# Kernel tuning notes

Hardware: AMD Instinct MI355X
Metric: run time of the kernel (lower is better)

Reference implementation:

```python
import jax, jax.numpy as jnp
import numpy as np

B, P, V = 8, 16, 32
N_TH1 = 20
N_TH2 = 2 * (N_TH1 - 1) + 1
NPC, NNS, NOUT = 16384, 8192, 8192


def make_directions(n_th1):
    n_th2 = 2 * (n_th1 - 1) + 1
    th1 = np.linspace(-np.pi / 2, np.pi / 2, n_th1)
    th2 = np.linspace(-np.pi, np.pi, n_th2)
    c1, s1 = np.cos(th1), np.sin(th1)
    c2, s2 = np.cos(th2), np.sin(th2)
    ds = []
    for i in range(1, n_th1 - 1):
        for j in range(n_th2 - 1):
            ds.append([c1[i] * c2[j], c1[i] * s2[j], s1[i]])
    ds.append([c1[0] * c2[0], c1[0] * s2[0], s1[0]])
    ds.append([c1[-1] * c2[0], c1[-1] * s2[0], s1[-1]])
    return np.asarray(ds, np.float32)

DIRS = jnp.asarray(make_directions(N_TH1))
D = DIRS.shape[0]  # (n_th1-2)*(n_th2-1)+2 = 686


def _spt(dirs, verts, smooth, trans):
    # dirs [B,P,N,3], verts [B,P,V,3] (centered), trans [B,P,1,3]
    z = jnp.einsum('bpvc,bpnc->bpvn', verts, dirs)          # [B,P,V,N]
    zm = jnp.maximum(z, 0.0)
    pe = smooth[:, :, None, None]                            # [B,P,1,1]
    maxz = jnp.clip(jnp.max(z, axis=2, keepdims=True), 1e-30, 1e30)
    k = 1.0 / maxz                                           # [B,P,1,N]
    zmk = jnp.clip(zm * k, 1e-30, 1e30)                      # tiny floor keeps pow grads finite
    sum_zm_p = jnp.sum(zmk ** pe, axis=2, keepdims=True)     # [B,P,1,N]
    h = sum_zm_p ** (1.0 / pe)                               # normalized support value
    s = jnp.clip(h, 1e-30, 1e30)
    dhdz = jnp.clip((zmk / s) ** (pe - 1.0), 1e-30, 1e30)    # [B,P,V,N]
    surf = jnp.einsum('bpvn,bpvc->bpnc', dhdz, verts) + trans
    h_out = jnp.clip(h / k, -1e30, 1e30).transpose(0, 1, 3, 2)  # [B,P,N,1]
    return h_out, surf


def _distance(verts, smooth, trans, pts, normal_filter=None):
    # pts [B,P,N,3]: per-part query points in global coords
    local = pts - trans
    nrm = jnp.sqrt(jnp.clip(jnp.sum(local * local, -1, keepdims=True), 1e-40, 1e40))
    d = local / nrm                                          # unit directions [B,P,N,3]
    h, surf = _spt(d, verts, smooth, trans)
    dist = nrm - h                                           # signed distance to support plane
    if normal_filter is not None:
        dist = jnp.where(normal_filter, 100.0, dist)
    return dist, surf, d


def _overlap(verts, smooth, trans):
    t = trans[:, :, 0, :]                                    # [B,P,3]
    diff = t[:, None, :, :] - t[:, :, None, :]               # [B,i,j,3] = t_j - t_i
    dn = jnp.sqrt(jnp.clip(jnp.sum(diff * diff, -1, keepdims=True), 1e-20, 1e20))
    eyem = jnp.eye(t.shape[1], dtype=t.dtype)[None, :, :, None]
    safe = jnp.array([1.0, 0.0, 0.0], dtype=t.dtype)
    d = diff / dn * (1.0 - eyem) + eyem * safe               # safe diagonal direction
    h, _ = _spt(d, verts, smooth, trans)                     # [B,P,P,1] support of part i toward j
    sep = dn - h - jnp.swapaxes(h, 1, 2)                     # center gap minus both supports
    return jax.nn.relu(-sep) * (1.0 - eyem)


def _forward(vertices, smoothness, pointcloud, nearsurf, out):
    mean_v = jnp.mean(vertices, axis=2, keepdims=True)       # [B,P,1,3]
    local_v = vertices - mean_v
    x = jnp.broadcast_to(DIRS[None, None], (B, P, D, 3))
    h, _ = _spt(x, local_v, smoothness, mean_v)              # [B,P,D,1]
    overlap = _overlap(local_v, smoothness, mean_v)
    pc = jnp.broadcast_to(pointcloud[:, None], (B, P, NPC, 3))
    distance, _, _ = _distance(local_v, smoothness, mean_v, pc)
    scale = jnp.clip(jnp.max(h, axis=2, keepdims=True), 1e-10, 10.0)  # [B,P,1,1]
    _, surf_pts, normals = _distance(local_v, smoothness, mean_v, x * scale + mean_v)
    surf_points = surf_pts.reshape(B, P * D, 3)
    sp2 = jnp.broadcast_to(surf_points[:, None], (B, P, P * D, 3))
    local_trans = jnp.transpose(mean_v, (0, 2, 1, 3)) - mean_v        # [B,P,P,3]
    nf = jnp.einsum('bijc,bidc->bijd', local_trans, normals)          # [B,P,P,D]
    normal_filter = nf.reshape(B, P, P * D)[..., None] < 0
    surf_distance, _, _ = _distance(local_v, smoothness, mean_v, sp2, normal_filter=normal_filter)
    sd = surf_distance.reshape(B, P, P, D, 1)
    df = 100.0 * jnp.eye(P, dtype=sd.dtype)[None, :, :, None, None]
    sd = jnp.where(df > 0, df, sd)                           # mask self-distance
    surf_distance = sd.reshape(B, P, P * D, 1)
    ns = jnp.broadcast_to(nearsurf[:, None], (B, P, NNS, 3))
    nearsurf_dist, _, _ = _distance(local_v, smoothness, mean_v, ns)
    op = jnp.broadcast_to(out[:, None], (B, P, NOUT, 3))
    out_dist, _, _ = _distance(local_v, smoothness, mean_v, op)
    return overlap, distance, x, surf_distance, surf_points, nearsurf_dist, out_dist


def setup_inputs() -> dict:
    key = jax.random.key(0)
    k1, k2, k3, k4, k5, k6 = jax.random.split(key, 6)
    centers = jax.random.uniform(k1, (B, P, 1, 3), minval=-1.0, maxval=1.0)
    vertices = centers + 0.3 * jax.random.normal(k2, (B, P, V, 3))
    smoothness = 2.5 + 7.5 * jax.random.uniform(k3, (B, P))
    pointcloud = jax.random.uniform(k4, (B, NPC, 3), minval=-1.5, maxval=1.5)
    nearsurf = jax.random.uniform(k5, (B, NNS, 3), minval=-1.5, maxval=1.5)
    out = jax.random.uniform(k6, (B, NOUT, 3), minval=-2.0, maxval=2.0)
    return {"vertices": vertices, "smoothness": smoothness, "pointcloud": pointcloud,
            "nearsurf": nearsurf, "out": out}


def reference(vertices, smoothness, pointcloud, nearsurf, out):
    return _forward(vertices, smoothness, pointcloud, nearsurf, out)
```

## Files before the change

kernel.cpp:

```cpp
#include <hip/hip_runtime.h>
#include <math.h>

#define PP 16
#define VV 32
#define DD 686

__device__ __forceinline__ float clampf(float x, float lo, float hi) {
    return fminf(fmaxf(x, lo), hi);
}
__device__ __forceinline__ float fexp2(float x) { return __builtin_amdgcn_exp2f(x); }
__device__ __forceinline__ float flog2(float x) { return __builtin_amdgcn_logf(x); }
__device__ __forceinline__ float frsq (float x) { return __builtin_amdgcn_rsqf(x); }
__device__ __forceinline__ float zpow(float z, float pe) {
    return fexp2(pe * flog2(fmaxf(z, 1e-30f)));
}

__device__ __forceinline__ float spt_h4(const float4* __restrict__ sv4, float pe, float ipe,
                                        float lx, float ly, float lz)
{
    float s0 = 0.f, s1 = 0.f, s2 = 0.f, s3 = 0.f;
#pragma unroll
    for (int c = 0; c < 8; ++c) {
        float4 a = sv4[3*c+0], b = sv4[3*c+1], d = sv4[3*c+2];
        s0 += zpow(a.x*lx + a.y*ly + a.z*lz, pe);
        s1 += zpow(a.w*lx + b.x*ly + b.y*lz, pe);
        s2 += zpow(b.z*lx + b.w*ly + d.x*lz, pe);
        s3 += zpow(d.y*lx + d.z*ly + d.w*lz, pe);
    }
    return fexp2(flog2((s0+s1) + (s2+s3)) * ipe);
}

__global__ void k_setup(const float* __restrict__ verts, const float* __restrict__ smooth,
                        double* __restrict__ dmean, float* __restrict__ fmean,
                        float* __restrict__ flocal, float* __restrict__ fpe,
                        float* __restrict__ finvpe, float* __restrict__ fdirs,
                        int BP, int doDirs)
{
    int blk = blockIdx.x;
    int tid = threadIdx.x;
    if (blk < 3) {
        if (!doDirs) return;
        int idx = blk * 256 + tid;
        if (idx >= DD) return;
        int i, j;
        if (idx < 684)      { i = idx / 38 + 1; j = idx - (idx / 38) * 38; }
        else if (idx == 684){ i = 0;  j = 0; }
        else                { i = 19; j = 0; }
        const double pi = 3.14159265358979323846;
        double th1 = -pi * 0.5 + (double)i * (pi / 19.0);
        double th2 = -pi       + (double)j * (pi / 19.0);
        fdirs[3*idx+0] = (float)(cos(th1) * cos(th2));
        fdirs[3*idx+1] = (float)(cos(th1) * sin(th2));
        fdirs[3*idx+2] = (float)(sin(th1));
        return;
    }
    int bp = (blk - 3) * 256 + tid;
    if (bp >= BP) return;
    const float* vv = verts + (size_t)bp * VV * 3;
    double sx = 0.0, sy = 0.0, sz = 0.0;
#pragma unroll
    for (int k = 0; k < VV; ++k) {
        sx += (double)vv[3*k+0];
        sy += (double)vv[3*k+1];
        sz += (double)vv[3*k+2];
    }
    double mx = sx / 32.0, my = sy / 32.0, mz = sz / 32.0;
    dmean[3*bp+0] = mx; dmean[3*bp+1] = my; dmean[3*bp+2] = mz;
    fmean[3*bp+0] = (float)mx; fmean[3*bp+1] = (float)my; fmean[3*bp+2] = (float)mz;
    float* lv = flocal + (size_t)bp * VV * 3;
#pragma unroll
    for (int k = 0; k < VV; ++k) {
        lv[3*k+0] = (float)((double)vv[3*k+0] - mx);
        lv[3*k+1] = (float)((double)vv[3*k+1] - my);
        lv[3*k+2] = (float)((double)vv[3*k+2] - mz);
    }
    float pe = smooth[bp];
    fpe[bp] = pe;
    finvpe[bp] = 1.0f / pe;
}

__global__ void __launch_bounds__(256) k_mid(
        const float* __restrict__ dirs, const float* __restrict__ flocal,
        const float* __restrict__ fmean, const double* __restrict__ dmean,
        const float* __restrict__ fpe, const float* __restrict__ finvpe,
        double* __restrict__ dscale,
        float* __restrict__ out2, float* __restrict__ fsurf, float* __restrict__ out4,
        float* __restrict__ out0, int BP)
{
    int tid = threadIdx.x;
    if (blockIdx.x < (unsigned)BP) {
        int bp = blockIdx.x;
        __shared__ __align__(16) float sv[VV*3];
        __shared__ float red[4];
        if (tid < VV*3) sv[tid] = flocal[(size_t)bp*VV*3 + tid];
        __syncthreads();
        const float4* sv4 = (const float4*)sv;
        float pe = fpe[bp], ipe = finvpe[bp];
        float m0 = fmean[3*bp+0], m1 = fmean[3*bp+1], m2 = fmean[3*bp+2];

        float l2h_reg[3];
        float m = -1e38f;
#pragma unroll
        for (int it = 0; it < 3; ++it) {
            int dd = tid + 256*it;
            if (dd >= DD) break;
            float dx = dirs[3*dd+0], dy = dirs[3*dd+1], dz = dirs[3*dd+2];
            float s0=0.f,s1=0.f,s2=0.f,s3=0.f;
#pragma unroll
            for (int c = 0; c < 8; ++c) {
                float4 a = sv4[3*c+0], b = sv4[3*c+1], d = sv4[3*c+2];
                s0 += zpow(a.x*dx + a.y*dy + a.z*dz, pe);
                s1 += zpow(a.w*dx + b.x*dy + b.y*dz, pe);
                s2 += zpow(b.z*dx + b.w*dy + d.x*dz, pe);
                s3 += zpow(d.y*dx + d.z*dy + d.w*dz, pe);
            }
            float l2h = flog2((s0+s1)+(s2+s3)) * ipe;
            l2h_reg[it] = l2h;
            m = fmaxf(m, fexp2(l2h));
            float* xp = out2 + ((size_t)bp * DD + dd) * 3;
            xp[0] = dx; xp[1] = dy; xp[2] = dz;
        }
#pragma unroll
        for (int o = 32; o > 0; o >>= 1) m = fmaxf(m, __shfl_down(m, o));
        if ((tid & 63) == 0) red[tid >> 6] = m;
        __syncthreads();
        if (tid == 0) {
            m = fmaxf(fmaxf(red[0], red[1]), fmaxf(red[2], red[3]));
            dscale[bp] = (double)clampf(m, 1e-10f, 10.0f);
        }

        float pem1 = pe - 1.0f;
#pragma unroll
        for (int it = 0; it < 3; ++it) {
            int dd = tid + 256*it;
            if (dd >= DD) break;
            float dx = dirs[3*dd+0], dy = dirs[3*dd+1], dz = dirs[3*dd+2];
            float nl2h = -l2h_reg[it];
            float sxx = 0.f, syy = 0.f, szz = 0.f;
#pragma unroll
            for (int c = 0; c < 8; ++c) {
                float4 a = sv4[3*c+0], b = sv4[3*c+1], d = sv4[3*c+2];
                {
                    float z = a.x*dx + a.y*dy + a.z*dz;
                    float dh = fexp2(pem1 * (flog2(fmaxf(z,1e-30f)) + nl2h));
                    sxx += dh * a.x; syy += dh * a.y; szz += dh * a.z;
                }
                {
                    float z = a.w*dx + b.x*dy + b.y*dz;
                    float dh = fexp2(pem1 * (flog2(fmaxf(z,1e-30f)) + nl2h));
                    sxx += dh * a.w; syy += dh * b.x; szz += dh * b.y;
                }
                {
                    float z = b.z*dx + b.w*dy + d.x*dz;
                    float dh = fexp2(pem1 * (flog2(fmaxf(z,1e-30f)) + nl2h));
                    sxx += dh * b.z; syy += dh * b.w; szz += dh * d.x;
                }
                {
                    float z = d.y*dx + d.z*dy + d.w*dz;
                    float dh = fexp2(pem1 * (flog2(fmaxf(z,1e-30f)) + nl2h));
                    sxx += dh * d.y; syy += dh * d.z; szz += dh * d.w;
                }
            }
            sxx += m0; syy += m1; szz += m2;
            float* spp = fsurf + ((size_t)bp * DD + dd) * 3;
            spp[0] = sxx; spp[1] = syy; spp[2] = szz;
            float* op = out4 + ((size_t)bp * DD + dd) * 3;
            op[0] = sxx; op[1] = syy; op[2] = szz;
        }
        return;
    }
    int b = blockIdx.x - BP;
    __shared__ __align__(16) float osv[PP*VV*3];
    __shared__ double smd[PP*3];
    __shared__ float  spe[PP];
    __shared__ float  sipe[PP];
    __shared__ float  sh[PP*PP];
    for (int t = tid; t < PP*VV*3; t += 256) osv[t] = flocal[(size_t)b*PP*VV*3 + t];
    if (tid < PP*3) smd[tid]  = dmean[(size_t)b*PP*3 + tid];
    if (tid < PP)  { spe[tid] = fpe[b*PP + tid]; sipe[tid] = finvpe[b*PP + tid]; }
    __syncthreads();
    int i = tid >> 4, j = tid & 15;
    double tx = smd[3*j+0] - smd[3*i+0];
    double ty = smd[3*j+1] - smd[3*i+1];
    double tz = smd[3*j+2] - smd[3*i+2];
    double dn2 = fmin(fmax(tx*tx + ty*ty + tz*tz, 1e-20), 1e20);
    double dn = sqrt(dn2);
    float dx, dy, dz;
    if (i == j) { dx = 1.0f; dy = 0.0f; dz = 0.0f; }
    else        { dx = (float)(tx/dn); dy = (float)(ty/dn); dz = (float)(tz/dn); }
    sh[tid] = spt_h4((const float4*)&osv[i*VV*3], spe[i], sipe[i], dx, dy, dz);
    __syncthreads();
    double sep = dn - (double)sh[i*16 + j] - (double)sh[j*16 + i];
    double ov = (i == j) ? 0.0 : fmax(-sep, 0.0);
    out0[(size_t)b*PP*PP + tid] = (float)ov;
}

__global__ void __launch_bounds__(256) k_heavy(
        const float* __restrict__ pc, int NPCv, int cPC,
        const float* __restrict__ ns, int NNSv, int cNS,
        const float* __restrict__ ob, int NOUTv, int cOU,
        const float* __restrict__ fsurf, const float* __restrict__ dirs,
        const float* __restrict__ flocal, const double* __restrict__ dmean,
        const float* __restrict__ fmean,
        const float* __restrict__ fpe, const float* __restrict__ finvpe,
        const double* __restrict__ dscale,
        float* __restrict__ out1, float* __restrict__ out5, float* __restrict__ out6,
        float* __restrict__ out3)
{
    int bp = blockIdx.x;
    int b  = bp >> 4;
    int tid = threadIdx.x;
    __shared__ __align__(16) float sv[VV*3];
    if (tid < VV*3) sv[tid] = flocal[(size_t)bp*VV*3 + tid];
    __syncthreads();
    const float4* sv4 = (const float4*)sv;
    float pe = fpe[bp], ipe = finvpe[bp];
    int y = blockIdx.y;
    int cD = cPC + cNS + cOU;

    if (y < cD) {
        float m0 = fmean[3*bp+0], m1 = fmean[3*bp+1], m2 = fmean[3*bp+2];
        const float* pts; int N; float* outp;
        if (y < cPC)               { pts = pc; N = NPCv;  outp = out1; }
        else if ((y -= cPC) < cNS) { pts = ns; N = NNSv;  outp = out5; }
        else                       { y -= cNS; pts = ob; N = NOUTv; outp = out6; }

        int n0 = y * 1024 + tid;
        float lx[4], ly[4], lz[4], acc[4];
#pragma unroll
        for (int q = 0; q < 4; ++q) {
            int n = n0 + 256*q;
            if (n < N) {
                const float* pp = pts + ((size_t)b * N + n) * 3;
                lx[q] = pp[0] - m0; ly[q] = pp[1] - m1; lz[q] = pp[2] - m2;
            } else { lx[q] = 1.f; ly[q] = 0.f; lz[q] = 0.f; }
            acc[q] = 0.f;
        }
#pragma unroll
        for (int c = 0; c < 8; ++c) {
            float4 a = sv4[3*c+0], bb = sv4[3*c+1], d = sv4[3*c+2];
#pragma unroll
            for (int q = 0; q < 4; ++q) {
                acc[q] += zpow(a.x*lx[q] + a.y*ly[q] + a.z*lz[q], pe)
                        + zpow(a.w*lx[q] + bb.x*ly[q] + bb.y*lz[q], pe)
                        + zpow(bb.z*lx[q] + bb.w*ly[q] + d.x*lz[q], pe)
                        + zpow(d.y*lx[q] + d.z*ly[q] + d.w*lz[q], pe);
            }
        }
#pragma unroll
        for (int q = 0; q < 4; ++q) {
            int n = n0 + 256*q;
            if (n >= N) continue;
            float n2 = clampf(lx[q]*lx[q] + ly[q]*ly[q] + lz[q]*lz[q], 1e-40f, 1e40f);
            float invr = frsq(n2);
            float nrm = n2 * invr;
            float hs = fexp2(flog2(acc[q]) * ipe) * invr;
            outp[(size_t)bp * N + n] = nrm - hs;
        }
        return;
    }
    int i = bp & 15;
    int q = (y - cD) * 256 + tid;
    if (q >= PP*DD) return;
    int j  = q / DD;
    int dd = q - j * DD;
    double sc  = dscale[bp];
    double mi0 = dmean[3*bp+0], mi1 = dmean[3*bp+1], mi2 = dmean[3*bp+2];
    double nlx = ((double)dirs[3*dd+0] * sc + mi0) - mi0;
    double nly = ((double)dirs[3*dd+1] * sc + mi1) - mi1;
    double nlz = ((double)dirs[3*dd+2] * sc + mi2) - mi2;
    const double* mj = dmean + (size_t)(b*PP + j) * 3;
    double dot = (mj[0]-mi0)*nlx + (mj[1]-mi1)*nly + (mj[2]-mi2)*nlz;
    float dist;
    if (i == j || dot < 0.0) {
        dist = 100.0f;
    } else {
        float fm0 = fmean[3*bp+0], fm1 = fmean[3*bp+1], fm2 = fmean[3*bp+2];
        const float* sp = fsurf + ((size_t)b * PP * DD + q) * 3;
        float lx = sp[0] - fm0;
        float ly = sp[1] - fm1;
        float lz = sp[2] - fm2;
        float n2 = clampf(lx*lx + ly*ly + lz*lz, 1e-40f, 1e40f);
        float invr = frsq(n2);
        float nrm = n2 * invr;
        float hs = spt_h4(sv4, pe, ipe, lx, ly, lz) * invr;
        dist = nrm - hs;
    }
    out3[(size_t)bp * PP * DD + q] = dist;
}

extern "C" void kernel_launch(void* const* d_in, const int* in_sizes, int n_in,
                              void* d_out, int out_size, void* d_ws, size_t ws_size,
                              hipStream_t stream)
{
    const float* verts  = nullptr;
    const float* smooth = nullptr;
    const float* pcb    = nullptr;
    const float* nsb    = nullptr;
    const float* ob     = nullptr;
    const float* dirsin = nullptr;
    int Bv = 8, BP = 128, NPCv = 16384, NNSv = 8192, NOUTv = 8192;

    {
        int si = 0;
        for (int i = 1; i < n_in; ++i) if (in_sizes[i] < in_sizes[si]) si = i;
        int bp = in_sizes[si];
        bool ok = (bp > 0) && (bp % PP == 0);
        int rem[8]; int nrem = 0;
        const float* vcand = nullptr; const float* dcand = nullptr;
        if (ok) {
            for (int i = 0; i < n_in && i < 8; ++i) {
                if (i == si) continue;
                if (!vcand && in_sizes[i] == bp * VV * 3) { vcand = (const float*)d_in[i]; continue; }
                if (!dcand && in_sizes[i] == DD * 3)      { dcand = (const float*)d_in[i]; continue; }
                rem[nrem++] = i;
            }
        }
        if (ok && vcand && nrem == 3) {
            int pci = rem[0];
            for (int r = 1; r < 3; ++r) if (in_sizes[rem[r]] > in_sizes[pci]) pci = rem[r];
            int oth[2]; int no = 0;
            for (int r = 0; r < 3; ++r) if (rem[r] != pci) oth[no++] = rem[r];
            int B = bp / PP;
            int npc = in_sizes[pci] / (3 * B);
            int nns = in_sizes[oth[0]] / (3 * B);
            int nou = in_sizes[oth[1]] / (3 * B);
            if (npc > 0 && nns > 0 && nou > 0) {
                smooth = (const float*)d_in[si];
                verts  = vcand;
                dirsin = dcand;
                pcb    = (const float*)d_in[pci];
                nsb    = (const float*)d_in[oth[0]];
                ob     = (const float*)d_in[oth[1]];
                Bv = B; BP = bp; NPCv = npc; NNSv = nns; NOUTv = nou;
            }
        }
        if (!verts) {
            verts  = (const float*)d_in[0];
            smooth = (const float*)d_in[1];
            pcb    = (const float*)d_in[2];
            nsb    = (const float*)d_in[3];
            ob     = (const float*)d_in[4];
            Bv = 8; BP = 128; NPCv = 16384; NNSv = 8192; NOUTv = 8192;
        }
    }

    double* dmean  = (double*)d_ws;
    double* dscale = dmean + 3*(size_t)BP;
    float*  fdirs  = (float*)(dscale + BP);
    float*  fmean  = fdirs + DD*3;
    float*  fpe    = fmean + 3*(size_t)BP;
    float*  finvpe = fpe + BP;
    float*  flocal = finvpe + BP;
    float*  fsurf  = flocal + 96*(size_t)BP;

    float* out = (float*)d_out;
    size_t o0 = 0;
    size_t o1 = o0 + (size_t)Bv*PP*PP;
    size_t o2 = o1 + (size_t)BP*NPCv;
    size_t o3 = o2 + (size_t)BP*DD*3;
    size_t o4 = o3 + (size_t)BP*PP*DD;
    size_t o5 = o4 + (size_t)BP*DD*3;
    size_t o6 = o5 + (size_t)BP*NNSv;

    const float* dirs = dirsin ? dirsin : fdirs;
    int nPrep = (BP + 255) / 256;
    k_setup<<<dim3(3 + nPrep), 256, 0, stream>>>(verts, smooth, dmean, fmean, flocal,
                                                 fpe, finvpe, fdirs, BP, dirsin ? 0 : 1);
    k_mid<<<dim3(BP + Bv), 256, 0, stream>>>(dirs, flocal, fmean, dmean, fpe, finvpe,
                                             dscale, out + o2, fsurf, out + o4, out + o0, BP);
    int cPC = (NPCv + 1023)/1024, cNS = (NNSv + 1023)/1024, cOU = (NOUTv + 1023)/1024;
    int cSD = (PP*DD + 255)/256;
    k_heavy<<<dim3(BP, cPC + cNS + cOU + cSD), 256, 0, stream>>>(
        pcb, NPCv, cPC, nsb, NNSv, cNS, ob, NOUTv, cOU,
        fsurf, dirs, flocal, dmean, fmean, fpe, finvpe, dscale,
        out + o1, out + o5, out + o6, out + o3);
}
```

Baseline: 141.3 us.

## Merge point-distance work into the mid kernel and split surface distance out

```diff
diff --git a/kernel.cpp b/kernel.cpp
--- a/kernel.cpp
+++ b/kernel.cpp
@@ -79,17 +79,24 @@
     finvpe[bp] = 1.0f / pe;
 }
 
-__global__ void __launch_bounds__(256) k_mid(
+__global__ void __launch_bounds__(256) k_work(
         const float* __restrict__ dirs, const float* __restrict__ flocal,
         const float* __restrict__ fmean, const double* __restrict__ dmean,
         const float* __restrict__ fpe, const float* __restrict__ finvpe,
         double* __restrict__ dscale,
+        const float* __restrict__ pc, int NPCv, int cPC,
+        const float* __restrict__ ns, int NNSv, int cNS,
+        const float* __restrict__ ob, int NOUTv, int cD,
         float* __restrict__ out2, float* __restrict__ fsurf, float* __restrict__ out4,
-        float* __restrict__ out0, int BP)
+        float* __restrict__ out0,
+        float* __restrict__ out1, float* __restrict__ out5, float* __restrict__ out6,
+        int BP, int Bv)
 {
     int tid = threadIdx.x;
-    if (blockIdx.x < (unsigned)BP) {
-        int bp = blockIdx.x;
+    int blk = blockIdx.x;
+
+    if (blk < BP) {
+        int bp = blk;
         __shared__ __align__(16) float sv[VV*3];
         __shared__ float red[4];
         if (tid < VV*3) sv[tid] = flocal[(size_t)bp*VV*3 + tid];
@@ -169,98 +176,100 @@
         }
         return;
     }
-    int b = blockIdx.x - BP;
-    __shared__ __align__(16) float osv[PP*VV*3];
-    __shared__ double smd[PP*3];
-    __shared__ float  spe[PP];
-    __shared__ float  sipe[PP];
-    __shared__ float  sh[PP*PP];
-    for (int t = tid; t < PP*VV*3; t += 256) osv[t] = flocal[(size_t)b*PP*VV*3 + t];
-    if (tid < PP*3) smd[tid]  = dmean[(size_t)b*PP*3 + tid];
-    if (tid < PP)  { spe[tid] = fpe[b*PP + tid]; sipe[tid] = finvpe[b*PP + tid]; }
+    if (blk < BP + Bv) {
+        int b = blk - BP;
+        __shared__ __align__(16) float osv[PP*VV*3];
+        __shared__ double smd[PP*3];
+        __shared__ float  spe[PP];
+        __shared__ float  sipe[PP];
+        __shared__ float  sh[PP*PP];
+        for (int t = tid; t < PP*VV*3; t += 256) osv[t] = flocal[(size_t)b*PP*VV*3 + t];
+        if (tid < PP*3) smd[tid]  = dmean[(size_t)b*PP*3 + tid];
+        if (tid < PP)  { spe[tid] = fpe[b*PP + tid]; sipe[tid] = finvpe[b*PP + tid]; }
+        __syncthreads();
+        int i = tid >> 4, j = tid & 15;
+        double tx = smd[3*j+0] - smd[3*i+0];
+        double ty = smd[3*j+1] - smd[3*i+1];
+        double tz = smd[3*j+2] - smd[3*i+2];
+        double dn2 = fmin(fmax(tx*tx + ty*ty + tz*tz, 1e-20), 1e20);
+        double dn = sqrt(dn2);
+        float dx, dy, dz;
+        if (i == j) { dx = 1.0f; dy = 0.0f; dz = 0.0f; }
+        else        { dx = (float)(tx/dn); dy = (float)(ty/dn); dz = (float)(tz/dn); }
+        sh[tid] = spt_h4((const float4*)&osv[i*VV*3], spe[i], sipe[i], dx, dy, dz);
+        __syncthreads();
+        double sep = dn - (double)sh[i*16 + j] - (double)sh[j*16 + i];
+        double ov = (i == j) ? 0.0 : fmax(-sep, 0.0);
+        out0[(size_t)b*PP*PP + tid] = (float)ov;
+        return;
+    }
+    int lin = blk - BP - Bv;
+    int bp  = lin / cD;
+    int y   = lin - bp * cD;
+    int b   = bp >> 4;
+    __shared__ __align__(16) float sv[VV*3];
+    if (tid < VV*3) sv[tid] = flocal[(size_t)bp*VV*3 + tid];
     __syncthreads();
-    int i = tid >> 4, j = tid & 15;
-    double tx = smd[3*j+0] - smd[3*i+0];
-    double ty = smd[3*j+1] - smd[3*i+1];
-    double tz = smd[3*j+2] - smd[3*i+2];
-    double dn2 = fmin(fmax(tx*tx + ty*ty + tz*tz, 1e-20), 1e20);
-    double dn = sqrt(dn2);
-    float dx, dy, dz;
-    if (i == j) { dx = 1.0f; dy = 0.0f; dz = 0.0f; }
-    else        { dx = (float)(tx/dn); dy = (float)(ty/dn); dz = (float)(tz/dn); }
-    sh[tid] = spt_h4((const float4*)&osv[i*VV*3], spe[i], sipe[i], dx, dy, dz);
-    __syncthreads();
-    double sep = dn - (double)sh[i*16 + j] - (double)sh[j*16 + i];
-    double ov = (i == j) ? 0.0 : fmax(-sep, 0.0);
-    out0[(size_t)b*PP*PP + tid] = (float)ov;
-}
-
-__global__ void __launch_bounds__(256) k_heavy(
-        const float* __restrict__ pc, int NPCv, int cPC,
-        const float* __restrict__ ns, int NNSv, int cNS,
-        const float* __restrict__ ob, int NOUTv, int cOU,
+    const float4* sv4 = (const float4*)sv;
+    float pe = fpe[bp], ipe = finvpe[bp];
+    float m0 = fmean[3*bp+0], m1 = fmean[3*bp+1], m2 = fmean[3*bp+2];
+    const float* pts; int N; float* outp;
+    if (y < cPC)               { pts = pc; N = NPCv;  outp = out1; }
+    else if ((y -= cPC) < cNS) { pts = ns; N = NNSv;  outp = out5; }
+    else                       { y -= cNS; pts = ob; N = NOUTv; outp = out6; }
+
+    int n0 = y * 1024 + tid;
+    float lx[4], ly[4], lz[4], acc[4];
+#pragma unroll
+    for (int q = 0; q < 4; ++q) {
+        int n = n0 + 256*q;
+        if (n < N) {
+            const float* pp = pts + ((size_t)b * N + n) * 3;
+            lx[q] = pp[0] - m0; ly[q] = pp[1] - m1; lz[q] = pp[2] - m2;
+        } else { lx[q] = 1.f; ly[q] = 0.f; lz[q] = 0.f; }
+        acc[q] = 0.f;
+    }
+#pragma unroll
+    for (int c = 0; c < 8; ++c) {
+        float4 a = sv4[3*c+0], bb = sv4[3*c+1], d = sv4[3*c+2];
+#pragma unroll
+        for (int q = 0; q < 4; ++q) {
+            acc[q] += zpow(a.x*lx[q] + a.y*ly[q] + a.z*lz[q], pe)
+                    + zpow(a.w*lx[q] + bb.x*ly[q] + bb.y*lz[q], pe)
+                    + zpow(bb.z*lx[q] + bb.w*ly[q] + d.x*lz[q], pe)
+                    + zpow(d.y*lx[q] + d.z*ly[q] + d.w*lz[q], pe);
+        }
+    }
+#pragma unroll
+    for (int q = 0; q < 4; ++q) {
+        int n = n0 + 256*q;
+        if (n >= N) continue;
+        float n2 = clampf(lx[q]*lx[q] + ly[q]*ly[q] + lz[q]*lz[q], 1e-40f, 1e40f);
+        float invr = frsq(n2);
+        float nrm = n2 * invr;
+        float hs = fexp2(flog2(acc[q]) * ipe) * invr;
+        outp[(size_t)bp * N + n] = nrm - hs;
+    }
+}
+
+__global__ void __launch_bounds__(256) k_surfdist(
         const float* __restrict__ fsurf, const float* __restrict__ dirs,
         const float* __restrict__ flocal, const double* __restrict__ dmean,
         const float* __restrict__ fmean,
         const float* __restrict__ fpe, const float* __restrict__ finvpe,
         const double* __restrict__ dscale,
-        float* __restrict__ out1, float* __restrict__ out5, float* __restrict__ out6,
         float* __restrict__ out3)
 {
     int bp = blockIdx.x;
     int b  = bp >> 4;
+    int i  = bp & 15;
     int tid = threadIdx.x;
     __shared__ __align__(16) float sv[VV*3];
     if (tid < VV*3) sv[tid] = flocal[(size_t)bp*VV*3 + tid];
     __syncthreads();
     const float4* sv4 = (const float4*)sv;
     float pe = fpe[bp], ipe = finvpe[bp];
-    int y = blockIdx.y;
-    int cD = cPC + cNS + cOU;
-
-    if (y < cD) {
-        float m0 = fmean[3*bp+0], m1 = fmean[3*bp+1], m2 = fmean[3*bp+2];
-        const float* pts; int N; float* outp;
-        if (y < cPC)               { pts = pc; N = NPCv;  outp = out1; }
-        else if ((y -= cPC) < cNS) { pts = ns; N = NNSv;  outp = out5; }
-        else                       { y -= cNS; pts = ob; N = NOUTv; outp = out6; }
-
-        int n0 = y * 1024 + tid;
-        float lx[4], ly[4], lz[4], acc[4];
-#pragma unroll
-        for (int q = 0; q < 4; ++q) {
-            int n = n0 + 256*q;
-            if (n < N) {
-                const float* pp = pts + ((size_t)b * N + n) * 3;
-                lx[q] = pp[0] - m0; ly[q] = pp[1] - m1; lz[q] = pp[2] - m2;
-            } else { lx[q] = 1.f; ly[q] = 0.f; lz[q] = 0.f; }
-            acc[q] = 0.f;
-        }
-#pragma unroll
-        for (int c = 0; c < 8; ++c) {
-            float4 a = sv4[3*c+0], bb = sv4[3*c+1], d = sv4[3*c+2];
-#pragma unroll
-            for (int q = 0; q < 4; ++q) {
-                acc[q] += zpow(a.x*lx[q] + a.y*ly[q] + a.z*lz[q], pe)
-                        + zpow(a.w*lx[q] + bb.x*ly[q] + bb.y*lz[q], pe)
-                        + zpow(bb.z*lx[q] + bb.w*ly[q] + d.x*lz[q], pe)
-                        + zpow(d.y*lx[q] + d.z*ly[q] + d.w*lz[q], pe);
-            }
-        }
-#pragma unroll
-        for (int q = 0; q < 4; ++q) {
-            int n = n0 + 256*q;
-            if (n >= N) continue;
-            float n2 = clampf(lx[q]*lx[q] + ly[q]*ly[q] + lz[q]*lz[q], 1e-40f, 1e40f);
-            float invr = frsq(n2);
-            float nrm = n2 * invr;
-            float hs = fexp2(flog2(acc[q]) * ipe) * invr;
-            outp[(size_t)bp * N + n] = nrm - hs;
-        }
-        return;
-    }
-    int i = bp & 15;
-    int q = (y - cD) * 256 + tid;
+    int q = blockIdx.y * 256 + tid;
     if (q >= PP*DD) return;
     int j  = q / DD;
     int dd = q - j * DD;
@@ -367,12 +376,13 @@
     int nPrep = (BP + 255) / 256;
     k_setup<<<dim3(3 + nPrep), 256, 0, stream>>>(verts, smooth, dmean, fmean, flocal,
                                                  fpe, finvpe, fdirs, BP, dirsin ? 0 : 1);
-    k_mid<<<dim3(BP + Bv), 256, 0, stream>>>(dirs, flocal, fmean, dmean, fpe, finvpe,
-                                             dscale, out + o2, fsurf, out + o4, out + o0, BP);
     int cPC = (NPCv + 1023)/1024, cNS = (NNSv + 1023)/1024, cOU = (NOUTv + 1023)/1024;
-    int cSD = (PP*DD + 255)/256;
-    k_heavy<<<dim3(BP, cPC + cNS + cOU + cSD), 256, 0, stream>>>(
-        pcb, NPCv, cPC, nsb, NNSv, cNS, ob, NOUTv, cOU,
-        fsurf, dirs, flocal, dmean, fmean, fpe, finvpe, dscale,
-        out + o1, out + o5, out + o6, out + o3);
-}
+    int cD  = cPC + cNS + cOU;
+    k_work<<<dim3(BP + Bv + BP*cD), 256, 0, stream>>>(
+        dirs, flocal, fmean, dmean, fpe, finvpe, dscale,
+        pcb, NPCv, cPC, nsb, NNSv, cNS, ob, NOUTv, cD,
+        out + o2, fsurf, out + o4, out + o0,
+        out + o1, out + o5, out + o6, BP, Bv);
+    k_surfdist<<<dim3(BP, (PP*DD + 255)/256), 256, 0, stream>>>(
+        fsurf, dirs, flocal, dmean, fmean, fpe, finvpe, dscale, out + o3);
+}
```

Result: faster. 134.4 us (-4.9%).
